# Kernel optimization log

Hardware: AMD Instinct MI355X
Metric: run time of the kernel (lower is better)

## Reference

```python
import jax, jax.numpy as jnp
import numpy as np

B, S, H, I, E = 2, 2048, 1024, 4096, 8


def setup_inputs() -> dict:
    key = jax.random.key(0)
    k1, k2, k3, k4 = jax.random.split(key, 4)
    hidden_states = jax.random.normal(k1, (B, S, H), dtype=jnp.float32)
    # router: nn.Linear(H, E, bias=False) -> weight (E, H)
    Wr = jax.random.normal(k2, (E, H), dtype=jnp.float32) * 0.02
    # per-expert MLP: Linear(H,I) weight (I,H); Linear(I,H) weight (H,I); stacked over E
    W1 = jax.random.normal(k3, (E, I, H), dtype=jnp.float32) * 0.02
    W2 = jax.random.normal(k4, (E, H, I), dtype=jnp.float32) * 0.02
    return {"hidden_states": hidden_states, "Wr": Wr, "W1": W1, "W2": W2}


def reference(hidden_states, Wr, W1, W2):
    b, s, h = hidden_states.shape
    n_exp = Wr.shape[0]
    x = hidden_states.reshape(-1, h)                      # (N, H)
    logits = x @ Wr.T                                     # (N, E)
    probs = jax.nn.softmax(logits, axis=-1)               # (N, E)
    # top_k with k == num_experts: sorted probs descending (one-hot mask then
    # covers every expert, so each expert sees every token; expert i's output is
    # weighted by the i-th largest prob, exactly as the torch code does).
    top_probs, _ = jax.lax.top_k(probs, n_exp)            # (N, E)
    hmid = jnp.einsum('nh,eih->nei', x, W1)               # (N, E, I)
    hmid = jax.nn.gelu(hmid, approximate=False)           # exact erf GELU (torch nn.GELU default)
    yexp = jnp.einsum('nei,ehi->neh', hmid, W2)           # (N, E, H)
    out = jnp.einsum('neh,ne->nh', yexp, top_probs)       # weighted combine
    return out.reshape(b, s, h)
```

## Files before the change

### kernel.cpp

```cpp
#include <hip/hip_runtime.h>
#include <hip/hip_bf16.h>

#define NTOK 4096
#define HD   1024
#define ID   4096
#define NE   8
#define LDH  (NE * ID)

typedef float  floatx4 __attribute__((ext_vector_type(4)));
typedef __bf16 bf16x8  __attribute__((ext_vector_type(8)));
typedef unsigned short u16;

__device__ __forceinline__ u16 f2bf(float f) {
    union { float f; unsigned int i; } c; c.f = f;
    return (u16)((c.i + 0x7fffu + ((c.i >> 16) & 1u)) >> 16);
}

__device__ __forceinline__ void async_copy16(u16* lds, const u16* g) {
    __builtin_amdgcn_global_load_lds(
        (const __attribute__((address_space(1))) void*)g,
        (__attribute__((address_space(3))) void*)lds, 16, 0, 0);
}

__device__ __forceinline__ float gelu_fast(float v) {
    const float u = v * (0.7978845608f + 0.0356774081f * v * v);
    const float t = 1.f - 2.f / (__expf(2.f * u) + 1.f);
    return 0.5f * v * (1.f + t);
}

#define FENCE()  asm volatile("" ::: "memory")
#define BAR()    do { FENCE(); __builtin_amdgcn_s_barrier(); FENCE(); } while (0)
#define WAITV4() asm volatile("s_waitcnt vmcnt(4)" ::: "memory")
#define WAITV0() asm volatile("s_waitcnt vmcnt(0)" ::: "memory")
#define WAITL0() asm volatile("s_waitcnt lgkmcnt(0)" ::: "memory")

__global__ __launch_bounds__(256) void convert_kernel(
    const float* __restrict__ src, u16* __restrict__ dst)
{
    const size_t i = ((size_t)blockIdx.x * 256 + threadIdx.x) * 8;
    const float4 a = *(const float4*)(src + i);
    const float4 b = *(const float4*)(src + i + 4);
    ushort4 o0, o1;
    o0.x = f2bf(a.x); o0.y = f2bf(a.y); o0.z = f2bf(a.z); o0.w = f2bf(a.w);
    o1.x = f2bf(b.x); o1.y = f2bf(b.y); o1.z = f2bf(b.z); o1.w = f2bf(b.w);
    *(ushort4*)(dst + i)     = o0;
    *(ushort4*)(dst + i + 4) = o1;
}

__global__ __launch_bounds__(256) void router_kernel(
    const float* __restrict__ x, const float* __restrict__ Wr,
    float* __restrict__ wbuf)
{
    const int n    = blockIdx.x * 4 + (threadIdx.x >> 6);
    const int lane = threadIdx.x & 63;
    const float* xr = x + (size_t)n * HD;
    float acc[NE];
#pragma unroll
    for (int e = 0; e < NE; ++e) acc[e] = 0.f;
    for (int h = lane; h < HD; h += 64) {
        const float xv = xr[h];
#pragma unroll
        for (int e = 0; e < NE; ++e) acc[e] += xv * Wr[e * HD + h];
    }
#pragma unroll
    for (int e = 0; e < NE; ++e) {
        float v = acc[e];
#pragma unroll
        for (int off = 32; off > 0; off >>= 1) v += __shfl_xor(v, off, 64);
        acc[e] = v;
    }
    float mx = acc[0];
#pragma unroll
    for (int e = 1; e < NE; ++e) mx = fmaxf(mx, acc[e]);
    float s = 0.f;
#pragma unroll
    for (int e = 0; e < NE; ++e) { acc[e] = __expf(acc[e] - mx); s += acc[e]; }
    const float inv = 1.f / s;
#pragma unroll
    for (int e = 0; e < NE; ++e) acc[e] *= inv;
#pragma unroll
    for (int i = 0; i < NE - 1; ++i)
#pragma unroll
        for (int j = 0; j < NE - 1 - i; ++j) {
            const float a = acc[j], b = acc[j + 1];
            acc[j] = fmaxf(a, b); acc[j + 1] = fminf(a, b);
        }
    if (lane < NE) wbuf[lane * NTOK + n] = acc[lane];
}

__device__ __forceinline__ void gemm256_tile(
    const u16* __restrict__ A, const u16* __restrict__ B,
    int ldA, int ldB, int K, int rowBase, int colBase,
    u16* As0, u16* As1, u16* Bs0, u16* Bs1,
    floatx4 acc[8][4])
{
    const int t    = threadIdx.x;
    const int w    = t >> 6, lane = t & 63;
    const int wm   = w & 1, wn = w >> 1;
    const int quad = lane >> 4, l15 = lane & 15;

    const int srow   = (w << 4) + (lane >> 2);
    const int schunk = ((lane & 3) ^ ((lane >> 3) & 3)) << 3;
    const u16* gA = A + (size_t)(rowBase + srow) * ldA + schunk;
    const u16* gB = B + (size_t)(colBase + srow) * ldB + schunk;
    const size_t hA = (size_t)128 * ldA, hB = (size_t)128 * ldB;
    u16* lA0 = As0 + w * 512;
    u16* lA1 = As1 + w * 512;
    u16* lB0 = Bs0 + w * 512;
    u16* lB1 = Bs1 + w * 512;

    const int sw = (l15 >> 1) & 3;
    int aoff[8], boff[4];
#pragma unroll
    for (int mi = 0; mi < 8; ++mi)
        aoff[mi] = (wm * 128 + mi * 16 + l15) * 32 + ((quad ^ sw) << 3);
#pragma unroll
    for (int ni = 0; ni < 4; ++ni)
        boff[ni] = (wn * 64 + ni * 16 + l15) * 32 + ((quad ^ sw) << 3);

#define STAGE2(lA, lB, kt) do { const int _ko = (kt) << 5;          \
        async_copy16(lA,        gA + _ko);                          \
        async_copy16(lA + 4096, gA + _ko + hA);                     \
        async_copy16(lB,        gB + _ko);                          \
        async_copy16(lB + 4096, gB + _ko + hB); } while (0)

    const int nkt = K >> 5;
    bf16x8 af[8], bfr[4];
    STAGE2(lA0, lB0, 0);
    STAGE2(lA1, lB1, 1);

#pragma unroll 1
    for (int kt = 0; kt < nkt; kt += 2) {
        WAITV4(); BAR();
#pragma unroll
        for (int mi = 0; mi < 8; ++mi) af[mi] = *(const bf16x8*)(As0 + aoff[mi]);
#pragma unroll
        for (int ni = 0; ni < 4; ++ni) bfr[ni] = *(const bf16x8*)(Bs0 + boff[ni]);
        WAITL0();
        __builtin_amdgcn_s_setprio(1);
#pragma unroll
        for (int mi = 0; mi < 4; ++mi)
#pragma unroll
            for (int ni = 0; ni < 4; ++ni)
                acc[mi][ni] = __builtin_amdgcn_mfma_f32_16x16x32_bf16(
                    af[mi], bfr[ni], acc[mi][ni], 0, 0, 0);
        __builtin_amdgcn_s_setprio(0);
        BAR();
        if (kt + 2 < nkt) STAGE2(lA0, lB0, kt + 2);
        __builtin_amdgcn_s_setprio(1);
#pragma unroll
        for (int mi = 4; mi < 8; ++mi)
#pragma unroll
            for (int ni = 0; ni < 4; ++ni)
                acc[mi][ni] = __builtin_amdgcn_mfma_f32_16x16x32_bf16(
                    af[mi], bfr[ni], acc[mi][ni], 0, 0, 0);
        __builtin_amdgcn_s_setprio(0);
        if (kt + 2 < nkt) { WAITV4(); } else { WAITV0(); }
        BAR();
#pragma unroll
        for (int mi = 0; mi < 8; ++mi) af[mi] = *(const bf16x8*)(As1 + aoff[mi]);
#pragma unroll
        for (int ni = 0; ni < 4; ++ni) bfr[ni] = *(const bf16x8*)(Bs1 + boff[ni]);
        WAITL0();
        __builtin_amdgcn_s_setprio(1);
#pragma unroll
        for (int mi = 0; mi < 4; ++mi)
#pragma unroll
            for (int ni = 0; ni < 4; ++ni)
                acc[mi][ni] = __builtin_amdgcn_mfma_f32_16x16x32_bf16(
                    af[mi], bfr[ni], acc[mi][ni], 0, 0, 0);
        __builtin_amdgcn_s_setprio(0);
        BAR();
        if (kt + 3 < nkt) STAGE2(lA1, lB1, kt + 3);
        __builtin_amdgcn_s_setprio(1);
#pragma unroll
        for (int mi = 4; mi < 8; ++mi)
#pragma unroll
            for (int ni = 0; ni < 4; ++ni)
                acc[mi][ni] = __builtin_amdgcn_mfma_f32_16x16x32_bf16(
                    af[mi], bfr[ni], acc[mi][ni], 0, 0, 0);
        __builtin_amdgcn_s_setprio(0);
    }
#undef STAGE2
}

__global__ __launch_bounds__(512, 2) void gemm1_kernel(
    const u16* __restrict__ X, const u16* __restrict__ W1b,
    const float* __restrict__ wbuf, u16* __restrict__ hmid)
{
    __shared__ __align__(16) u16 As[2][8192];
    __shared__ __align__(16) u16 Bs[2][8192];
    floatx4 acc[8][4] = {};
    const int bid = blockIdx.x;
    const int swz = (bid & 7) * 256 + (bid >> 3);
    const int mt = swz >> 7, nt = swz & 127;
    const int rowBase = mt * 256, colBase = nt * 256;
    const int e = colBase >> 12;

    gemm256_tile(X, W1b, HD, HD, HD, rowBase, colBase,
                 As[0], As[1], Bs[0], Bs[1], acc);

    const int t = threadIdx.x, w = t >> 6, lane = t & 63;
    const int wm = w & 1, wn = w >> 1, quad = lane >> 4, l15 = lane & 15;
#pragma unroll
    for (int mi = 0; mi < 8; ++mi)
#pragma unroll
        for (int r = 0; r < 4; ++r) {
            const int row = rowBase + wm * 128 + mi * 16 + quad * 4 + r;
            const float wv = wbuf[e * NTOK + row];
#pragma unroll
            for (int ni = 0; ni < 4; ++ni) {
                const int col = colBase + wn * 64 + ni * 16 + l15;
                hmid[(size_t)row * LDH + col] =
                    f2bf(gelu_fast(acc[mi][ni][r]) * wv);
            }
        }
}

__global__ __launch_bounds__(512, 2) void gemm2_kernel(
    const u16* __restrict__ hmid, const u16* __restrict__ W2b,
    float* __restrict__ accbuf)
{
    __shared__ __align__(16) u16 As[2][8192];
    __shared__ __align__(16) u16 Bs[2][8192];
    floatx4 acc[8][4] = {};
    const int bid = blockIdx.x;
    const int swz = (bid & 7) * 32 + (bid >> 3);
    const int z = swz >> 6, mt = (swz >> 2) & 15, nt = swz & 3;
    const int rowBase = mt * 256, colBase = nt * 256;

    for (int ee = 0; ee < 2; ++ee) {
        const int e = 2 * z + ee;
        gemm256_tile(hmid + (size_t)e * ID, W2b + (size_t)e * HD * ID,
                     LDH, ID, ID, rowBase, colBase,
                     As[0], As[1], Bs[0], Bs[1], acc);
    }

    float* accs = accbuf + (size_t)z * NTOK * HD;
    const int t = threadIdx.x, w = t >> 6, lane = t & 63;
    const int wm = w & 1, wn = w >> 1, quad = lane >> 4, l15 = lane & 15;
#pragma unroll
    for (int mi = 0; mi < 8; ++mi)
#pragma unroll
        for (int r = 0; r < 4; ++r) {
            const int row = rowBase + wm * 128 + mi * 16 + quad * 4 + r;
#pragma unroll
            for (int ni = 0; ni < 4; ++ni) {
                const int col = colBase + wn * 64 + ni * 16 + l15;
                accs[(size_t)row * HD + col] = acc[mi][ni][r];
            }
        }
}

__global__ __launch_bounds__(256) void finalize_kernel(
    const float* __restrict__ accbuf, float* __restrict__ out)
{
    const size_t NH = (size_t)NTOK * HD;
    const size_t i = ((size_t)blockIdx.x * 256 + threadIdx.x) * 4;
    const float4 a = *(const float4*)(accbuf + i);
    const float4 b = *(const float4*)(accbuf + NH + i);
    const float4 c = *(const float4*)(accbuf + 2 * NH + i);
    const float4 d = *(const float4*)(accbuf + 3 * NH + i);
    float4 o;
    o.x = a.x + b.x + c.x + d.x; o.y = a.y + b.y + c.y + d.y;
    o.z = a.z + b.z + c.z + d.z; o.w = a.w + b.w + c.w + d.w;
    *(float4*)(out + i) = o;
}

extern "C" void kernel_launch(void* const* d_in, const int* in_sizes, int n_in,
                              void* d_out, int out_size, void* d_ws, size_t ws_size,
                              hipStream_t stream) {
    const float* x  = (const float*)d_in[0];
    const float* Wr = (const float*)d_in[1];
    const float* W1 = (const float*)d_in[2];
    const float* W2 = (const float*)d_in[3];
    float* out = (float*)d_out;

    const size_t MB = 1024 * 1024;
    char* ws = (char*)d_ws;
    float* wbuf   = (float*)ws;
    u16*   Xb     = (u16*)(ws + 131072);
    u16*   W1b    = (u16*)(ws + 131072 + 8 * MB);
    u16*   W2b    = (u16*)(ws + 131072 + 72 * MB);
    u16*   hmid   = (u16*)(ws + 131072 + 136 * MB);
    float* accbuf = (float*)(ws + 131072 + 392 * MB);
    if (ws_size < 131072 + 456 * MB) return;

    convert_kernel<<<dim3((NTOK * HD) / 2048), 256, 0, stream>>>(x, Xb);
    convert_kernel<<<dim3((NE * ID * HD) / 2048), 256, 0, stream>>>(W1, W1b);
    convert_kernel<<<dim3((NE * HD * ID) / 2048), 256, 0, stream>>>(W2, W2b);
    router_kernel<<<dim3(NTOK / 4), 256, 0, stream>>>(x, Wr, wbuf);

    gemm1_kernel<<<dim3(NE * ID / 256 * (NTOK / 256)), 512, 0, stream>>>(
        Xb, W1b, wbuf, hmid);
    gemm2_kernel<<<dim3((NTOK / 256) * (HD / 256) * 4), 512, 0, stream>>>(
        hmid, W2b, accbuf);
    finalize_kernel<<<dim3(NTOK * HD / 1024), 256, 0, stream>>>(accbuf, out);
}
```

Before: 974.1 us.

## Split gemm2 per expert, merge weight converts, defer LDS wait in MFMA loop

gemm2 now launches one block per expert tile (512 blocks instead of 256), writing eight partial sums that finalize reduces. This gives more blocks to fill the CUs. Reusing the workspace start (including wbuf/Xb) for the low partials is safe because those buffers are dead by then. The W1 and W2 bf16 conversions are merged into one launch. In the GEMM loop the lgkmcnt wait moves after the first MFMA half, and B fragments load first, relying on compiler-inserted waits. The cost is extra partial-sum traffic in finalize.

```diff
diff --git a/kernel.cpp b/kernel.cpp
--- a/kernel.cpp
+++ b/kernel.cpp
@@ -43,6 +43,24 @@
     ushort4 o0, o1;
     o0.x = f2bf(a.x); o0.y = f2bf(a.y); o0.z = f2bf(a.z); o0.w = f2bf(a.w);
     o1.x = f2bf(b.x); o1.y = f2bf(b.y); o1.z = f2bf(b.z); o1.w = f2bf(b.w);
+    *(ushort4*)(dst + i)     = o0;
+    *(ushort4*)(dst + i + 4) = o1;
+}
+
+__global__ __launch_bounds__(256) void convert2_kernel(
+    const float* __restrict__ s1, u16* __restrict__ d1,
+    const float* __restrict__ s2, u16* __restrict__ d2, int half)
+{
+    const int b = blockIdx.x;
+    const float* src = (b < half) ? s1 : s2;
+    u16*         dst = (b < half) ? d1 : d2;
+    const int    bb  = (b < half) ? b : b - half;
+    const size_t i = ((size_t)bb * 256 + threadIdx.x) * 8;
+    const float4 a = *(const float4*)(src + i);
+    const float4 c = *(const float4*)(src + i + 4);
+    ushort4 o0, o1;
+    o0.x = f2bf(a.x); o0.y = f2bf(a.y); o0.z = f2bf(a.z); o0.w = f2bf(a.w);
+    o1.x = f2bf(c.x); o1.y = f2bf(c.y); o1.z = f2bf(c.z); o1.w = f2bf(c.w);
     *(ushort4*)(dst + i)     = o0;
     *(ushort4*)(dst + i + 4) = o1;
 }
@@ -133,10 +151,9 @@
     for (int kt = 0; kt < nkt; kt += 2) {
         WAITV4(); BAR();
 #pragma unroll
+        for (int ni = 0; ni < 4; ++ni) bfr[ni] = *(const bf16x8*)(Bs0 + boff[ni]);
+#pragma unroll
         for (int mi = 0; mi < 8; ++mi) af[mi] = *(const bf16x8*)(As0 + aoff[mi]);
-#pragma unroll
-        for (int ni = 0; ni < 4; ++ni) bfr[ni] = *(const bf16x8*)(Bs0 + boff[ni]);
-        WAITL0();
         __builtin_amdgcn_s_setprio(1);
 #pragma unroll
         for (int mi = 0; mi < 4; ++mi)
@@ -145,6 +162,7 @@
                 acc[mi][ni] = __builtin_amdgcn_mfma_f32_16x16x32_bf16(
                     af[mi], bfr[ni], acc[mi][ni], 0, 0, 0);
         __builtin_amdgcn_s_setprio(0);
+        WAITL0();
         BAR();
         if (kt + 2 < nkt) STAGE2(lA0, lB0, kt + 2);
         __builtin_amdgcn_s_setprio(1);
@@ -158,10 +176,9 @@
         if (kt + 2 < nkt) { WAITV4(); } else { WAITV0(); }
         BAR();
 #pragma unroll
+        for (int ni = 0; ni < 4; ++ni) bfr[ni] = *(const bf16x8*)(Bs1 + boff[ni]);
+#pragma unroll
         for (int mi = 0; mi < 8; ++mi) af[mi] = *(const bf16x8*)(As1 + aoff[mi]);
-#pragma unroll
-        for (int ni = 0; ni < 4; ++ni) bfr[ni] = *(const bf16x8*)(Bs1 + boff[ni]);
-        WAITL0();
         __builtin_amdgcn_s_setprio(1);
 #pragma unroll
         for (int mi = 0; mi < 4; ++mi)
@@ -170,6 +187,7 @@
                 acc[mi][ni] = __builtin_amdgcn_mfma_f32_16x16x32_bf16(
                     af[mi], bfr[ni], acc[mi][ni], 0, 0, 0);
         __builtin_amdgcn_s_setprio(0);
+        WAITL0();
         BAR();
         if (kt + 3 < nkt) STAGE2(lA1, lB1, kt + 3);
         __builtin_amdgcn_s_setprio(1);
@@ -219,24 +237,23 @@
 
 __global__ __launch_bounds__(512, 2) void gemm2_kernel(
     const u16* __restrict__ hmid, const u16* __restrict__ W2b,
-    float* __restrict__ accbuf)
+    float* __restrict__ acclo, float* __restrict__ acchi)
 {
     __shared__ __align__(16) u16 As[2][8192];
     __shared__ __align__(16) u16 Bs[2][8192];
     floatx4 acc[8][4] = {};
     const int bid = blockIdx.x;
-    const int swz = (bid & 7) * 32 + (bid >> 3);
+    const int swz = (bid & 7) * 64 + (bid >> 3);
     const int z = swz >> 6, mt = (swz >> 2) & 15, nt = swz & 3;
     const int rowBase = mt * 256, colBase = nt * 256;
 
-    for (int ee = 0; ee < 2; ++ee) {
-        const int e = 2 * z + ee;
-        gemm256_tile(hmid + (size_t)e * ID, W2b + (size_t)e * HD * ID,
-                     LDH, ID, ID, rowBase, colBase,
-                     As[0], As[1], Bs[0], Bs[1], acc);
-    }
-
-    float* accs = accbuf + (size_t)z * NTOK * HD;
+    gemm256_tile(hmid + (size_t)z * ID, W2b + (size_t)z * HD * ID,
+                 LDH, ID, ID, rowBase, colBase,
+                 As[0], As[1], Bs[0], Bs[1], acc);
+
+    const size_t NH = (size_t)NTOK * HD;
+    float* accs = (z < 4) ? (acclo + (size_t)z * NH)
+                          : (acchi + (size_t)(z - 4) * NH);
     const int t = threadIdx.x, w = t >> 6, lane = t & 63;
     const int wm = w & 1, wn = w >> 1, quad = lane >> 4, l15 = lane & 15;
 #pragma unroll
@@ -253,17 +270,22 @@
 }
 
 __global__ __launch_bounds__(256) void finalize_kernel(
-    const float* __restrict__ accbuf, float* __restrict__ out)
+    const float* __restrict__ acclo, const float* __restrict__ acchi,
+    float* __restrict__ out)
 {
     const size_t NH = (size_t)NTOK * HD;
     const size_t i = ((size_t)blockIdx.x * 256 + threadIdx.x) * 4;
-    const float4 a = *(const float4*)(accbuf + i);
-    const float4 b = *(const float4*)(accbuf + NH + i);
-    const float4 c = *(const float4*)(accbuf + 2 * NH + i);
-    const float4 d = *(const float4*)(accbuf + 3 * NH + i);
-    float4 o;
-    o.x = a.x + b.x + c.x + d.x; o.y = a.y + b.y + c.y + d.y;
-    o.z = a.z + b.z + c.z + d.z; o.w = a.w + b.w + c.w + d.w;
+    float4 o = *(const float4*)(acclo + i);
+#pragma unroll
+    for (int z = 1; z < 4; ++z) {
+        const float4 a = *(const float4*)(acclo + (size_t)z * NH + i);
+        o.x += a.x; o.y += a.y; o.z += a.z; o.w += a.w;
+    }
+#pragma unroll
+    for (int z = 0; z < 4; ++z) {
+        const float4 a = *(const float4*)(acchi + (size_t)z * NH + i);
+        o.x += a.x; o.y += a.y; o.z += a.z; o.w += a.w;
+    }
     *(float4*)(out + i) = o;
 }
 
@@ -283,17 +305,19 @@
     u16*   W1b    = (u16*)(ws + 131072 + 8 * MB);
     u16*   W2b    = (u16*)(ws + 131072 + 72 * MB);
     u16*   hmid   = (u16*)(ws + 131072 + 136 * MB);
-    float* accbuf = (float*)(ws + 131072 + 392 * MB);
+    float* acclo  = (float*)ws;
+    float* acchi  = (float*)(ws + 131072 + 392 * MB);
     if (ws_size < 131072 + 456 * MB) return;
 
     convert_kernel<<<dim3((NTOK * HD) / 2048), 256, 0, stream>>>(x, Xb);
-    convert_kernel<<<dim3((NE * ID * HD) / 2048), 256, 0, stream>>>(W1, W1b);
-    convert_kernel<<<dim3((NE * HD * ID) / 2048), 256, 0, stream>>>(W2, W2b);
+    convert2_kernel<<<dim3(2 * (NE * ID * HD) / 2048), 256, 0, stream>>>(
+        W1, W1b, W2, W2b, (NE * ID * HD) / 2048);
     router_kernel<<<dim3(NTOK / 4), 256, 0, stream>>>(x, Wr, wbuf);
 
     gemm1_kernel<<<dim3(NE * ID / 256 * (NTOK / 256)), 512, 0, stream>>>(
         Xb, W1b, wbuf, hmid);
-    gemm2_kernel<<<dim3((NTOK / 256) * (HD / 256) * 4), 512, 0, stream>>>(
-        hmid, W2b, accbuf);
-    finalize_kernel<<<dim3(NTOK * HD / 1024), 256, 0, stream>>>(accbuf, out);
-}
+    gemm2_kernel<<<dim3((NTOK / 256) * (HD / 256) * 8), 512, 0, stream>>>(
+        hmid, W2b, acclo, acchi);
+    finalize_kernel<<<dim3(NTOK * HD / 1024), 256, 0, stream>>>(
+        acclo, acchi, out);
+}
```

After: 1.014 ms. 4.1% more time.
